# Performance work log

Hardware: AMD Instinct MI355X
Metric: run time of the kernel (lower is better)

## Reference

```python
import jax, jax.numpy as jnp
import numpy as np
from jax import lax

STRIDE = (1, 1)
PADDING = ((1, 1), (1, 1))
DILATION = (1, 1)


def setup_inputs() -> dict:
    key = jax.random.key(0)
    k1, k2, k3, k4 = jax.random.split(key, 4)
    bs, cin, h, w = 64, 128, 56, 56
    k_exp, cout, kh, kw = 8, 128, 3, 3
    x = jax.random.normal(k1, (bs, cin, h, w), dtype=jnp.float32)
    routing_weight = jax.random.uniform(k2, (bs, k_exp), dtype=jnp.float32)
    weight = jax.random.normal(k3, (k_exp, cout, cin, kh, kw), dtype=jnp.float32) * (1.0 / np.sqrt(cin * kh * kw))
    bias = jax.random.normal(k4, (k_exp, cout), dtype=jnp.float32) * 0.01
    return {"x": x, "routing_weight": routing_weight, "weight": weight, "bias": bias}


def reference(x, routing_weight, weight, bias):
    # CondConv combine_kernel path: per-sample kernel = routing-weighted sum of experts,
    # then a standard conv per sample (equivalent to torch groups=bs trick).
    # w_mix: [bs, oc, c, kh, kw]
    w_mix = jnp.einsum('bk,kocij->bocij', routing_weight, weight)
    b_mix = routing_weight @ bias  # [bs, oc]

    def conv_one(xi, wi):
        # xi: [c, h, w], wi: [oc, c, kh, kw]
        return lax.conv_general_dilated(
            xi[None], wi,
            window_strides=STRIDE,
            padding=PADDING,
            rhs_dilation=DILATION,
            dimension_numbers=('NCHW', 'OIHW', 'NCHW'),
        )[0]  # [oc, oh, ow]

    out = jax.vmap(conv_one)(x, w_mix)  # [bs, oc, oh, ow]
    out = out + b_mix[:, :, None, None]
    return out
```

## Files before the change

kernel.cpp:

```cpp
#include <hip/hip_runtime.h>

#define BS    64
#define CIN   128
#define OCH   128
#define HW    56
#define KEXP  8
#define KTOT  1152
#define NSTEP 36
#define CELLE 40
#define ROWE  (58 * CELLE)
#define PLANEE (58 * ROWE)
#define WMIX_PS (NSTEP * OCH * 32)
#define SLAB_CHUNKS 1160
#define BUFE 10240

typedef __bf16 bf16x8 __attribute__((ext_vector_type(8)));
typedef float  f32x4  __attribute__((ext_vector_type(4)));

__device__ __forceinline__ unsigned f2bf(float f) {
    union { float f; unsigned u; } v; v.f = f;
    unsigned r = v.u + 0x7fffu + ((v.u >> 16) & 1u);
    return r >> 16;
}

__device__ __forceinline__ void gl16(const unsigned short* g, unsigned short* l) {
    __builtin_amdgcn_global_load_lds(
        (const __attribute__((address_space(1))) void*)g,
        (__attribute__((address_space(3))) void*)l, 16, 0, 0);
}

__global__ __launch_bounds__(256) void prep_xt(const float* __restrict__ x,
                                               unsigned short* __restrict__ xt) {
    __shared__ unsigned short t[CIN * HW];
    int b = blockIdx.x, ihp = blockIdx.y;
    int tid = threadIdx.x;
    bool border = (ihp == 0) || (ihp == 57);
    if (!border) {
        int ih = ihp - 1;
        const float* xr = x + (size_t)b * CIN * HW * HW + (size_t)ih * HW;
        for (int i = tid; i < CIN * 28; i += 256) {
            int c = i / 28, w2 = i - c * 28;
            float2 v = *(const float2*)(xr + (size_t)c * (HW * HW) + w2 * 2);
            unsigned pk = f2bf(v.x) | (f2bf(v.y) << 16);
            *(unsigned*)&t[c * HW + w2 * 2] = pk;
        }
    }
    __syncthreads();
    for (int j = tid; j < 4 * 58 * 5; j += 256) {
        int q = j / 290, rr = j - q * 290;
        int cell = rr / 5, p = rr - cell * 5;
        union { unsigned short u[8]; uint4 v; } o;
        o.v = make_uint4(0u, 0u, 0u, 0u);
        if (!border && p < 4 && cell >= 1 && cell <= 56) {
            #pragma unroll
            for (int k = 0; k < 8; ++k)
                o.u[k] = t[(q * 32 + p * 8 + k) * HW + (cell - 1)];
        }
        *(uint4*)&xt[((size_t)(b * 4 + q) * 3364 + (size_t)ihp * 58) * CELLE
                     + cell * CELLE + p * 8] = o.v;
    }
}

__global__ __launch_bounds__(256) void prep_wmix(
        const float* __restrict__ rw, const float* __restrict__ wgt,
        unsigned short* __restrict__ wmix) {
    __shared__ float wlds[KEXP * KTOT];
    __shared__ float rwl[16 * KEXP];
    int oc  = blockIdx.x;
    int bg  = blockIdx.y;
    int tid = threadIdx.x;

    if (tid < 16 * KEXP) rwl[tid] = rw[bg * 16 * KEXP + tid];
    const float* wsrc = wgt + (size_t)oc * KTOT;
    #pragma unroll
    for (int e = 0; e < KEXP; ++e) {
        const float* we = wsrc + (size_t)e * OCH * KTOT;
        for (int j = tid; j < KTOT; j += 256) wlds[e * KTOT + j] = we[j];
    }
    __syncthreads();

    for (int t = tid; t < KTOT; t += 256) {
        int c = t & 127, rs = t >> 7;
        int q = c >> 5, cl = c & 31;
        size_t oidx = ((size_t)(q * 9 + rs) * OCH + oc) * 32 + cl;
        float w8[KEXP];
        #pragma unroll
        for (int e = 0; e < KEXP; ++e) w8[e] = wlds[e * KTOT + c * 9 + rs];
        #pragma unroll
        for (int b = 0; b < 16; ++b) {
            float a = 0.f;
            #pragma unroll
            for (int e = 0; e < KEXP; ++e) a += rwl[b * KEXP + e] * w8[e];
            wmix[(size_t)(bg * 16 + b) * WMIX_PS + oidx] = (unsigned short)f2bf(a);
        }
    }
}

__global__ __launch_bounds__(256) void prep_bmix(
        const float* __restrict__ rw, const float* __restrict__ bias,
        float* __restrict__ bmix) {
    int i = blockIdx.x * 256 + threadIdx.x;
    int b = i >> 7, oc = i & 127;
    float a = 0.f;
    #pragma unroll
    for (int e = 0; e < KEXP; ++e) a += rw[b * KEXP + e] * bias[e * OCH + oc];
    bmix[i] = a;
}

__global__ __launch_bounds__(256, 4) void condconv_mfma(
        const unsigned short* __restrict__ xt, const unsigned short* __restrict__ wmix,
        const float* __restrict__ bmix, float* __restrict__ out) {
    __shared__ unsigned short patch[2][BUFE];

    int blk  = blockIdx.x;
    int b    = blk & 63;
    int tile = blk >> 6;
    int oh0  = tile * 2;
    int tid  = threadIdx.x;
    int wave = tid >> 6, lane = tid & 63, ln = lane & 15, quad = lane >> 4;

    const unsigned short* ap = wmix + (size_t)b * WMIX_PS
                             + (size_t)(wave * 32 + ln) * 32 + quad * 8;

    const unsigned short* xbase = xt + (size_t)(b * 4) * PLANEE + (size_t)oh0 * ROWE;
    int g[5];
    #pragma unroll
    for (int i = 0; i < 5; ++i) {
        int gi = wave * 320 + i * 64 + lane;
        g[i] = (gi < SLAB_CHUNKS) ? gi : (SLAB_CHUNKS - 1);
    }

    int cb[7], offn[7];
    #pragma unroll
    for (int nt = 0; nt < 7; ++nt) {
        int n   = nt * 16 + ln;
        int row = (n >= 56) ? 1 : 0;
        int ow  = n - row * 56;
        cb[nt]   = (row * 58 + ow) * CELLE + quad * 8;
        offn[nt] = (oh0 + row) * HW + ow;
    }

    f32x4 acc[2][7] = {};

    auto stage = [&](int q, int bf) {
        const unsigned short* sq = xbase + (size_t)q * PLANEE;
        unsigned short* l0 = &patch[bf][0] + wave * 2560;
        #pragma unroll
        for (int i = 0; i < 5; ++i)
            gl16(sq + (size_t)g[i] * 8, l0 + i * 512);
    };

    stage(0, 0);
    bf16x8 pa0[2], pa1[2];
    pa0[0] = *(const bf16x8*)(ap);
    pa1[0] = *(const bf16x8*)(ap + 512);
    pa0[1] = *(const bf16x8*)(ap + 4096);
    pa1[1] = *(const bf16x8*)(ap + 4096 + 512);
    __syncthreads();

    #pragma unroll
    for (int q = 0; q < 4; ++q) {
        if (q < 3) stage(q + 1, (q + 1) & 1);
        #pragma unroll
        for (int s9 = 0; s9 < 9; ++s9) {
            const int s = q * 9 + s9;
            bf16x8 ca0 = pa0[s & 1], ca1 = pa1[s & 1];
            const int sp = (s + 2 < NSTEP) ? (s + 2) : (NSTEP - 1);
            pa0[s & 1] = *(const bf16x8*)(ap + (size_t)sp * 4096);
            pa1[s & 1] = *(const bf16x8*)(ap + (size_t)sp * 4096 + 512);
            const int r = s9 / 3, sc = s9 - r * 3;
            const int pshift = (r * 58 + sc) * CELLE;
            #pragma unroll
            for (int nt = 0; nt < 7; ++nt) {
                bf16x8 bb = *(const bf16x8*)&patch[q & 1][cb[nt] + pshift];
                acc[0][nt] = __builtin_amdgcn_mfma_f32_16x16x32_bf16(ca0, bb, acc[0][nt], 0, 0, 0);
                acc[1][nt] = __builtin_amdgcn_mfma_f32_16x16x32_bf16(ca1, bb, acc[1][nt], 0, 0, 0);
            }
        }
        __syncthreads();
    }

    const float* bmb = bmix + b * OCH;
    float* ob = out + (size_t)b * OCH * HW * HW;
    #pragma unroll
    for (int mt = 0; mt < 2; ++mt) {
        #pragma unroll
        for (int rg = 0; rg < 4; ++rg) {
            int oc = wave * 32 + mt * 16 + quad * 4 + rg;
            float bv = bmb[oc];
            #pragma unroll
            for (int nt = 0; nt < 7; ++nt)
                ob[(size_t)oc * (HW * HW) + offn[nt]] = acc[mt][nt][rg] + bv;
        }
    }
}

extern "C" void kernel_launch(void* const* d_in, const int* in_sizes, int n_in,
                              void* d_out, int out_size, void* d_ws, size_t ws_size,
                              hipStream_t stream) {
    (void)in_sizes; (void)n_in; (void)out_size; (void)ws_size;
    const float* x    = (const float*)d_in[0];
    const float* rw   = (const float*)d_in[1];
    const float* wgt  = (const float*)d_in[2];
    const float* bias = (const float*)d_in[3];
    float* outp = (float*)d_out;

    unsigned short* wmix = (unsigned short*)d_ws;
    float* bmix = (float*)((char*)d_ws + (size_t)BS * WMIX_PS * 2);
    unsigned short* xtw = (unsigned short*)((char*)d_ws + (size_t)BS * WMIX_PS * 2 + 32768);

    hipLaunchKernelGGL(prep_xt,   dim3(BS, 58), dim3(256), 0, stream, x, xtw);
    hipLaunchKernelGGL(prep_wmix, dim3(OCH, 4), dim3(256), 0, stream, rw, wgt, wmix);
    hipLaunchKernelGGL(prep_bmix, dim3(32),     dim3(256), 0, stream, rw, bias, bmix);
    hipLaunchKernelGGL(condconv_mfma, dim3(BS * 28), dim3(256), 0, stream,
                       xtw, wmix, bmix, outp);
}
```

Baseline: 274.9 us.

## Fuse preprocessing kernels into one launch and compute bias mix in epilogue

Merges the input transpose/convert and expert weight mixing into a single heterogeneous-block launch, and removes the separate bias-mix kernel by computing the routed bias inside the conv epilogue. The input transpose now reads global memory directly with strided per-channel loads instead of staging through LDS. Conv staging uses a flat thread-to-chunk mapping and a smaller LDS buffer. The goals are fewer launches and less LDS use per block, at the cost of less coalesced reads in the transpose path and the 36 KB weight-mix LDS footprint now also being allocated by transpose blocks.

Result: slower. 291.1 us (+5.9%).

```diff
diff --git a/kernel.cpp b/kernel.cpp
--- a/kernel.cpp
+++ b/kernel.cpp
@@ -12,7 +12,8 @@
 #define PLANEE (58 * ROWE)
 #define WMIX_PS (NSTEP * OCH * 32)
 #define SLAB_CHUNKS 1160
-#define BUFE 10240
+#define BUFE (SLAB_CHUNKS * 8)
+#define XT_BLOCKS (BS * 58)
 
 typedef __bf16 bf16x8 __attribute__((ext_vector_type(8)));
 typedef float  f32x4  __attribute__((ext_vector_type(4)));
@@ -29,87 +30,66 @@
         (__attribute__((address_space(3))) void*)l, 16, 0, 0);
 }
 
-__global__ __launch_bounds__(256) void prep_xt(const float* __restrict__ x,
-                                               unsigned short* __restrict__ xt) {
-    __shared__ unsigned short t[CIN * HW];
-    int b = blockIdx.x, ihp = blockIdx.y;
-    int tid = threadIdx.x;
-    bool border = (ihp == 0) || (ihp == 57);
-    if (!border) {
-        int ih = ihp - 1;
-        const float* xr = x + (size_t)b * CIN * HW * HW + (size_t)ih * HW;
-        for (int i = tid; i < CIN * 28; i += 256) {
-            int c = i / 28, w2 = i - c * 28;
-            float2 v = *(const float2*)(xr + (size_t)c * (HW * HW) + w2 * 2);
-            unsigned pk = f2bf(v.x) | (f2bf(v.y) << 16);
-            *(unsigned*)&t[c * HW + w2 * 2] = pk;
-        }
-    }
-    __syncthreads();
-    for (int j = tid; j < 4 * 58 * 5; j += 256) {
-        int q = j / 290, rr = j - q * 290;
-        int cell = rr / 5, p = rr - cell * 5;
-        union { unsigned short u[8]; uint4 v; } o;
-        o.v = make_uint4(0u, 0u, 0u, 0u);
-        if (!border && p < 4 && cell >= 1 && cell <= 56) {
-            #pragma unroll
-            for (int k = 0; k < 8; ++k)
-                o.u[k] = t[(q * 32 + p * 8 + k) * HW + (cell - 1)];
-        }
-        *(uint4*)&xt[((size_t)(b * 4 + q) * 3364 + (size_t)ihp * 58) * CELLE
-                     + cell * CELLE + p * 8] = o.v;
-    }
-}
-
-__global__ __launch_bounds__(256) void prep_wmix(
-        const float* __restrict__ rw, const float* __restrict__ wgt,
-        unsigned short* __restrict__ wmix) {
+__global__ __launch_bounds__(256) void prep_fused(
+        const float* __restrict__ x, const float* __restrict__ rw,
+        const float* __restrict__ wgt,
+        unsigned short* __restrict__ xt, unsigned short* __restrict__ wmix) {
     __shared__ float wlds[KEXP * KTOT];
     __shared__ float rwl[16 * KEXP];
-    int oc  = blockIdx.x;
-    int bg  = blockIdx.y;
+    int blk = blockIdx.x;
     int tid = threadIdx.x;
 
-    if (tid < 16 * KEXP) rwl[tid] = rw[bg * 16 * KEXP + tid];
-    const float* wsrc = wgt + (size_t)oc * KTOT;
-    #pragma unroll
-    for (int e = 0; e < KEXP; ++e) {
-        const float* we = wsrc + (size_t)e * OCH * KTOT;
-        for (int j = tid; j < KTOT; j += 256) wlds[e * KTOT + j] = we[j];
-    }
-    __syncthreads();
-
-    for (int t = tid; t < KTOT; t += 256) {
-        int c = t & 127, rs = t >> 7;
-        int q = c >> 5, cl = c & 31;
-        size_t oidx = ((size_t)(q * 9 + rs) * OCH + oc) * 32 + cl;
-        float w8[KEXP];
+    if (blk < XT_BLOCKS) {
+        int b = blk / 58, ihp = blk - b * 58;
+        bool border = (ihp == 0) || (ihp == 57);
+        const float* xb = x + (size_t)b * CIN * HW * HW + (size_t)(ihp - 1) * HW;
+        for (int j = tid; j < 4 * 58 * 5; j += 256) {
+            int q = j / 290, rr = j - q * 290;
+            int cell = rr / 5, p = rr - cell * 5;
+            union { unsigned short u[8]; uint4 v; } o;
+            o.v = make_uint4(0u, 0u, 0u, 0u);
+            if (!border && p < 4 && cell >= 1 && cell <= 56) {
+                const float* src = xb + (size_t)(q * 32 + p * 8) * (HW * HW) + (cell - 1);
+                #pragma unroll
+                for (int k = 0; k < 8; ++k)
+                    o.u[k] = (unsigned short)f2bf(src[(size_t)k * (HW * HW)]);
+            }
+            *(uint4*)&xt[((size_t)(b * 4 + q)) * PLANEE + (size_t)ihp * ROWE
+                         + cell * CELLE + p * 8] = o.v;
+        }
+    } else {
+        int wb = blk - XT_BLOCKS;
+        int oc = wb & 127, bg = wb >> 7;
+        if (tid < 16 * KEXP) rwl[tid] = rw[bg * 16 * KEXP + tid];
+        const float* wsrc = wgt + (size_t)oc * KTOT;
         #pragma unroll
-        for (int e = 0; e < KEXP; ++e) w8[e] = wlds[e * KTOT + c * 9 + rs];
-        #pragma unroll
-        for (int b = 0; b < 16; ++b) {
-            float a = 0.f;
+        for (int e = 0; e < KEXP; ++e) {
+            const float* we = wsrc + (size_t)e * OCH * KTOT;
+            for (int j = tid; j < KTOT; j += 256) wlds[e * KTOT + j] = we[j];
+        }
+        __syncthreads();
+        for (int t = tid; t < KTOT; t += 256) {
+            int c = t & 127, rs = t >> 7;
+            int q = c >> 5, cl = c & 31;
+            size_t oidx = ((size_t)(q * 9 + rs) * OCH + oc) * 32 + cl;
+            float w8[KEXP];
             #pragma unroll
-            for (int e = 0; e < KEXP; ++e) a += rwl[b * KEXP + e] * w8[e];
-            wmix[(size_t)(bg * 16 + b) * WMIX_PS + oidx] = (unsigned short)f2bf(a);
+            for (int e = 0; e < KEXP; ++e) w8[e] = wlds[e * KTOT + c * 9 + rs];
+            #pragma unroll
+            for (int b = 0; b < 16; ++b) {
+                float a = 0.f;
+                #pragma unroll
+                for (int e = 0; e < KEXP; ++e) a += rwl[b * KEXP + e] * w8[e];
+                wmix[(size_t)(bg * 16 + b) * WMIX_PS + oidx] = (unsigned short)f2bf(a);
+            }
         }
     }
 }
 
-__global__ __launch_bounds__(256) void prep_bmix(
-        const float* __restrict__ rw, const float* __restrict__ bias,
-        float* __restrict__ bmix) {
-    int i = blockIdx.x * 256 + threadIdx.x;
-    int b = i >> 7, oc = i & 127;
-    float a = 0.f;
-    #pragma unroll
-    for (int e = 0; e < KEXP; ++e) a += rw[b * KEXP + e] * bias[e * OCH + oc];
-    bmix[i] = a;
-}
-
 __global__ __launch_bounds__(256, 4) void condconv_mfma(
         const unsigned short* __restrict__ xt, const unsigned short* __restrict__ wmix,
-        const float* __restrict__ bmix, float* __restrict__ out) {
+        const float* __restrict__ rw, const float* __restrict__ bias,
+        float* __restrict__ out) {
     __shared__ unsigned short patch[2][BUFE];
 
     int blk  = blockIdx.x;
@@ -123,12 +103,6 @@
                              + (size_t)(wave * 32 + ln) * 32 + quad * 8;
 
     const unsigned short* xbase = xt + (size_t)(b * 4) * PLANEE + (size_t)oh0 * ROWE;
-    int g[5];
-    #pragma unroll
-    for (int i = 0; i < 5; ++i) {
-        int gi = wave * 320 + i * 64 + lane;
-        g[i] = (gi < SLAB_CHUNKS) ? gi : (SLAB_CHUNKS - 1);
-    }
 
     int cb[7], offn[7];
     #pragma unroll
@@ -144,10 +118,12 @@
 
     auto stage = [&](int q, int bf) {
         const unsigned short* sq = xbase + (size_t)q * PLANEE;
-        unsigned short* l0 = &patch[bf][0] + wave * 2560;
         #pragma unroll
-        for (int i = 0; i < 5; ++i)
-            gl16(sq + (size_t)g[i] * 8, l0 + i * 512);
+        for (int it = 0; it < 5; ++it) {
+            int ci = it * 256 + tid;
+            if (ci < SLAB_CHUNKS)
+                gl16(sq + (size_t)ci * 8, &patch[bf][0] + (size_t)ci * 8);
+        }
     };
 
     stage(0, 0);
@@ -180,14 +156,18 @@
         __syncthreads();
     }
 
-    const float* bmb = bmix + b * OCH;
+    float rwr[KEXP];
+    #pragma unroll
+    for (int e = 0; e < KEXP; ++e) rwr[e] = rw[b * KEXP + e];
     float* ob = out + (size_t)b * OCH * HW * HW;
     #pragma unroll
     for (int mt = 0; mt < 2; ++mt) {
         #pragma unroll
         for (int rg = 0; rg < 4; ++rg) {
             int oc = wave * 32 + mt * 16 + quad * 4 + rg;
-            float bv = bmb[oc];
+            float bv = 0.f;
+            #pragma unroll
+            for (int e = 0; e < KEXP; ++e) bv += rwr[e] * bias[e * OCH + oc];
             #pragma unroll
             for (int nt = 0; nt < 7; ++nt)
                 ob[(size_t)oc * (HW * HW) + offn[nt]] = acc[mt][nt][rg] + bv;
@@ -206,12 +186,10 @@
     float* outp = (float*)d_out;
 
     unsigned short* wmix = (unsigned short*)d_ws;
-    float* bmix = (float*)((char*)d_ws + (size_t)BS * WMIX_PS * 2);
-    unsigned short* xtw = (unsigned short*)((char*)d_ws + (size_t)BS * WMIX_PS * 2 + 32768);
+    unsigned short* xtw  = (unsigned short*)((char*)d_ws + (size_t)BS * WMIX_PS * 2);
 
-    hipLaunchKernelGGL(prep_xt,   dim3(BS, 58), dim3(256), 0, stream, x, xtw);
-    hipLaunchKernelGGL(prep_wmix, dim3(OCH, 4), dim3(256), 0, stream, rw, wgt, wmix);
-    hipLaunchKernelGGL(prep_bmix, dim3(32),     dim3(256), 0, stream, rw, bias, bmix);
+    hipLaunchKernelGGL(prep_fused, dim3(XT_BLOCKS + OCH * 4), dim3(256), 0, stream,
+                       x, rw, wgt, xtw, wmix);
     hipLaunchKernelGGL(condconv_mfma, dim3(BS * 28), dim3(256), 0, stream,
-                       xtw, wmix, bmix, outp);
+                       xtw, wmix, rw, bias, outp);
 }
```
